# Kernel tuning notes

Hardware: AMD Instinct MI355X
Metric: run time of the kernel (lower is better)

Reference implementation:

```python
import jax, jax.numpy as jnp
import numpy as np

B, C, H, W = 64, 1, 1024, 1024
G, K, S = 64, 3, 2
HG0, HL = 512, 512
D_IN = K * G * G * C  # 12288


def setup_inputs() -> dict:
    key = jax.random.key(0)
    k1, k2, k3, k4, k5, k6 = jax.random.split(key, 6)
    x = jax.random.normal(k1, (B, C, H, W), dtype=jnp.float32)
    l_t_prev = jax.random.uniform(k2, (B, 2), dtype=jnp.float32, minval=-1.0, maxval=1.0)
    W1 = jax.random.normal(k3, (HG0, D_IN), dtype=jnp.float32) * 0.02
    W2 = jax.random.normal(k4, (HL, 2), dtype=jnp.float32) * 0.02
    W3 = jax.random.normal(k5, (HG0 + HL, HG0), dtype=jnp.float32) * 0.02
    W4 = jax.random.normal(k6, (HG0 + HL, HL), dtype=jnp.float32) * 0.02
    return {"x": x, "l_t_prev": l_t_prev, "W1": W1, "W2": W2, "W3": W3, "W4": W4}


def _extract_patch(x, coords, size):
    """Crop a size x size window per sample, centered at coords, zero-padded OOB,
    then avg-pool by factor size//G down to (B, C, G, G)."""
    r = size // G
    P = size // 2 + 1  # padding used by the torch code; makes every slice in-bounds
    xp = jnp.pad(x, ((0, 0), (0, 0), (P, P), (P, P)))
    sy = coords[:, 1] - size // 2 + P
    sx = coords[:, 0] - size // 2 + P

    def one(im, y0, x0):
        return jax.lax.dynamic_slice(im, (0, y0, x0), (C, size, size))

    p = jax.vmap(one)(xp, sy, sx)  # (B, C, size, size)
    if r > 1:
        p = p.reshape(B, C, G, r, G, r).mean(axis=(3, 5))  # avg_pool2d(kernel=r)
    return p


def _foveate(x, l):
    # denormalize: coords in [0, H], truncated to int
    coords = (0.5 * ((l + 1.0) * H)).astype(jnp.int32)  # (B, 2) as [x, y]
    patches = []
    size = G * S ** (K - 1)
    for _ in range(K):
        patches.append(_extract_patch(x, coords, size))  # (B, 1, G, G)
        size = size // S
    return jnp.concatenate(patches, axis=1)  # (B, K, G, G)


def reference(x, l_t_prev, W1, W2, W3, W4):
    phi = _foveate(x, l_t_prev)                      # (B, K, G, G)
    phi_flat = phi.reshape(phi.shape[0], -1)         # (B, K*G*G)
    h = jax.nn.leaky_relu(phi_flat @ W1.T)           # (B, HG0)
    l_out = jax.nn.leaky_relu(l_t_prev @ W2.T)       # computed but unused (as in source)
    what = h @ W3.T                                  # (B, HG0+HL)
    where = h @ W4.T                                 # fc4 applied to phi features (source quirk)
    g_t = jax.nn.leaky_relu(what + where)
    return g_t
```

## Files before the change

kernel.cpp:

```cpp
#include <hip/hip_runtime.h>
#include <hip/hip_bf16.h>

#define B_N 64
#define D_IN 12288
#define HG0 512
#define OUT_N 1024

#define KC1 16
#define DBLOCK1 768
#define DWAVE1 192

typedef __attribute__((ext_vector_type(8))) short bf16x8;
typedef __attribute__((ext_vector_type(4))) float f32x4;

static __device__ __forceinline__ short f2bf(float f) {
  __hip_bfloat16 h = __float2bfloat16(f);
  return *reinterpret_cast<short*>(&h);
}

__global__ __launch_bounds__(256) void foveate_kernel(
    const float* __restrict__ x, const float* __restrict__ l,
    short* __restrict__ phi) {
  int idx = blockIdx.x * 256 + threadIdx.x;
  int b = idx / D_IN;
  int d = idx - b * D_IN;
  int k = d >> 12;
  int rem = d & 4095;
  int gy = rem >> 6, gx = rem & 63;

  float lx = l[b * 2 + 0];
  float ly = l[b * 2 + 1];
  int cx = (int)(0.5f * ((lx + 1.0f) * 1024.0f));
  int cy = (int)(0.5f * ((ly + 1.0f) * 1024.0f));

  const float* xb = x + ((size_t)b << 20);
  float v;

  if (k == 0) {
    int y0 = cy - 128 + gy * 4;
    int x0 = cx - 128 + gx * 4;
    float s = 0.0f;
    #pragma unroll
    for (int dy = 0; dy < 4; ++dy) {
      int yy = y0 + dy;
      if ((unsigned)yy < 1024u) {
        const float* row = xb + ((size_t)yy << 10);
        #pragma unroll
        for (int dx = 0; dx < 4; ++dx) {
          int xx = x0 + dx;
          if ((unsigned)xx < 1024u) s += row[xx];
        }
      }
    }
    v = s * 0.0625f;
  } else if (k == 1) {
    int y0 = cy - 64 + gy * 2;
    int x0 = cx - 64 + gx * 2;
    float s = 0.0f;
    #pragma unroll
    for (int dy = 0; dy < 2; ++dy) {
      int yy = y0 + dy;
      if ((unsigned)yy < 1024u) {
        const float* row = xb + ((size_t)yy << 10);
        #pragma unroll
        for (int dx = 0; dx < 2; ++dx) {
          int xx = x0 + dx;
          if ((unsigned)xx < 1024u) s += row[xx];
        }
      }
    }
    v = s * 0.25f;
  } else {
    int yy = cy - 32 + gy;
    int xx = cx - 32 + gx;
    v = 0.0f;
    if ((unsigned)yy < 1024u && (unsigned)xx < 1024u) v = xb[((size_t)yy << 10) + xx];
  }
  phi[idx] = f2bf(v);
}

__global__ __launch_bounds__(256) void gemm1_kernel(
    const short* __restrict__ phi, const float* __restrict__ W1,
    float* __restrict__ partial1) {
  __shared__ float lds[4 * 16 * 64];
  int wave = threadIdx.x >> 6;
  int lane = threadIdx.x & 63;
  int lc = lane & 15;
  int kg = lane >> 4;
  int j0 = blockIdx.x * 16;
  int dbase = blockIdx.y * DBLOCK1 + wave * DWAVE1;

  f32x4 acc[4] = {{0,0,0,0},{0,0,0,0},{0,0,0,0},{0,0,0,0}};

  const float* wrow = W1 + (size_t)(j0 + lc) * D_IN + kg * 8;
  const short* prow = phi + kg * 8;

  #pragma unroll
  for (int ks = 0; ks < DWAVE1 / 32; ++ks) {
    int d0 = dbase + ks * 32;
    float4 wa = *(const float4*)(wrow + d0);
    float4 wb = *(const float4*)(wrow + d0 + 4);
    bf16x8 af;
    af[0] = f2bf(wa.x); af[1] = f2bf(wa.y); af[2] = f2bf(wa.z); af[3] = f2bf(wa.w);
    af[4] = f2bf(wb.x); af[5] = f2bf(wb.y); af[6] = f2bf(wb.z); af[7] = f2bf(wb.w);
    #pragma unroll
    for (int t = 0; t < 4; ++t) {
      bf16x8 bf = *(const bf16x8*)(prow + (size_t)(t * 16 + lc) * D_IN + d0);
      acc[t] = __builtin_amdgcn_mfma_f32_16x16x32_bf16(af, bf, acc[t], 0, 0, 0);
    }
  }

  #pragma unroll
  for (int t = 0; t < 4; ++t)
    #pragma unroll
    for (int r = 0; r < 4; ++r)
      lds[wave * 1024 + (kg * 4 + r) * 64 + t * 16 + lc] = acc[t][r];
  __syncthreads();

  float* pp = partial1 + (size_t)blockIdx.y * (HG0 * 64) + (size_t)j0 * 64;
  #pragma unroll
  for (int i = 0; i < 4; ++i) {
    int e = threadIdx.x + 256 * i;
    float s = lds[e] + lds[1024 + e] + lds[2048 + e] + lds[3072 + e];
    pp[e] = s;
  }
}

__global__ __launch_bounds__(256) void reduce1_kernel(
    const float* __restrict__ partial1, short* __restrict__ h) {
  int idx = blockIdx.x * 256 + threadIdx.x;
  float s = 0.0f;
  #pragma unroll
  for (int kc = 0; kc < KC1; ++kc) s += partial1[(size_t)kc * (HG0 * 64) + idx];
  float v = (s >= 0.0f) ? s : 0.01f * s;
  int j = idx >> 6, b = idx & 63;
  h[(size_t)b * HG0 + j] = f2bf(v);
}

__global__ __launch_bounds__(256) void gemm2_kernel(
    const short* __restrict__ h, const float* __restrict__ W3,
    const float* __restrict__ W4, float* __restrict__ out) {
  __shared__ float lds[4 * 1024];
  int wave = threadIdx.x >> 6;
  int lane = threadIdx.x & 63;
  int lc = lane & 15;
  int kg = lane >> 4;
  int o0 = blockIdx.x * 16;
  int jbase = wave * 128;

  f32x4 acc[4] = {{0,0,0,0},{0,0,0,0},{0,0,0,0},{0,0,0,0}};

  #pragma unroll
  for (int ks = 0; ks < 4; ++ks) {
    int j0 = jbase + ks * 32;
    const float* w3r = W3 + (size_t)(o0 + lc) * HG0 + j0 + kg * 8;
    const float* w4r = W4 + (size_t)(o0 + lc) * HG0 + j0 + kg * 8;
    float4 a3 = *(const float4*)w3r;
    float4 b3 = *(const float4*)(w3r + 4);
    float4 a4 = *(const float4*)w4r;
    float4 b4 = *(const float4*)(w4r + 4);
    bf16x8 bf;
    bf[0] = f2bf(a3.x + a4.x); bf[1] = f2bf(a3.y + a4.y);
    bf[2] = f2bf(a3.z + a4.z); bf[3] = f2bf(a3.w + a4.w);
    bf[4] = f2bf(b3.x + b4.x); bf[5] = f2bf(b3.y + b4.y);
    bf[6] = f2bf(b3.z + b4.z); bf[7] = f2bf(b3.w + b4.w);
    #pragma unroll
    for (int t = 0; t < 4; ++t) {
      bf16x8 af = *(const bf16x8*)(h + (size_t)(t * 16 + lc) * HG0 + j0 + kg * 8);
      acc[t] = __builtin_amdgcn_mfma_f32_16x16x32_bf16(af, bf, acc[t], 0, 0, 0);
    }
  }

  #pragma unroll
  for (int t = 0; t < 4; ++t)
    #pragma unroll
    for (int r = 0; r < 4; ++r)
      lds[wave * 1024 + t * 256 + kg * 64 + r * 16 + lc] = acc[t][r];
  __syncthreads();

  #pragma unroll
  for (int i = 0; i < 4; ++i) {
    int e = threadIdx.x + 256 * i;
    float s = lds[e] + lds[1024 + e] + lds[2048 + e] + lds[3072 + e];
    float v = (s >= 0.0f) ? s : 0.01f * s;
    int b = ((e >> 8) << 4) + (((e >> 6) & 3) << 2) + ((e >> 4) & 3);
    out[(size_t)b * OUT_N + o0 + (e & 15)] = v;
  }
}

extern "C" void kernel_launch(void* const* d_in, const int* in_sizes, int n_in,
                              void* d_out, int out_size, void* d_ws, size_t ws_size,
                              hipStream_t stream) {
  const float* x  = (const float*)d_in[0];
  const float* l  = (const float*)d_in[1];
  const float* W1 = (const float*)d_in[2];
  const float* W3 = (const float*)d_in[4];
  const float* W4 = (const float*)d_in[5];
  float* out = (float*)d_out;

  char* ws = (char*)d_ws;
  short* phi      = (short*)(ws);
  float* partial1 = (float*)(ws + (1u << 21));
  short* h        = (short*)(ws + (1u << 21) + (1u << 22));

  foveate_kernel<<<dim3((B_N * D_IN) / 256), dim3(256), 0, stream>>>(x, l, phi);
  gemm1_kernel<<<dim3(32, KC1), dim3(256), 0, stream>>>(phi, W1, partial1);
  reduce1_kernel<<<dim3((HG0 * 64) / 256), dim3(256), 0, stream>>>(partial1, h);
  gemm2_kernel<<<dim3(OUT_N / 16), dim3(256), 0, stream>>>(h, W3, W4, out);
}
```

Measured before the change: 34.36 us.

## Fuse split-K reduction into gemm1 via atomic counter, precombine W3+W4 in prep

The separate reduce kernel is removed. The last gemm1 block to finish each output tile, detected with an atomic counter and thread fences, now sums the split-K partials and writes the leaky-relu bf16 h. W3+W4 is summed and converted to bf16 once, inside the foveate launch, so gemm2 reads half the bytes and does no conversion. Split-K is doubled to 32 to put more blocks in flight, which doubles the partial traffic and adds the serial reduction tail in the last block of each tile.

```diff
diff --git a/kernel.cpp b/kernel.cpp
--- a/kernel.cpp
+++ b/kernel.cpp
@@ -6,9 +6,12 @@
 #define HG0 512
 #define OUT_N 1024
 
-#define KC1 16
-#define DBLOCK1 768
-#define DWAVE1 192
+#define KC1 32
+#define DBLOCK1 384
+#define DWAVE1 96
+
+#define NFOV 3072
+#define NW34 512
 
 typedef __attribute__((ext_vector_type(8))) short bf16x8;
 typedef __attribute__((ext_vector_type(4))) float f32x4;
@@ -18,10 +21,24 @@
   return *reinterpret_cast<short*>(&h);
 }
 
-__global__ __launch_bounds__(256) void foveate_kernel(
+__global__ __launch_bounds__(256) void prep_kernel(
     const float* __restrict__ x, const float* __restrict__ l,
-    short* __restrict__ phi) {
-  int idx = blockIdx.x * 256 + threadIdx.x;
+    const float* __restrict__ W3, const float* __restrict__ W4,
+    short* __restrict__ phi, short* __restrict__ w34, int* __restrict__ cnt) {
+  int bx = blockIdx.x;
+  if (bx >= NFOV) {
+    int e = (bx - NFOV) * 1024 + threadIdx.x * 4;
+    float4 a = *(const float4*)(W3 + e);
+    float4 b = *(const float4*)(W4 + e);
+    short4 o;
+    o.x = f2bf(a.x + b.x); o.y = f2bf(a.y + b.y);
+    o.z = f2bf(a.z + b.z); o.w = f2bf(a.w + b.w);
+    *(short4*)(w34 + e) = o;
+    if (bx == NFOV && threadIdx.x < 32) cnt[threadIdx.x] = 0;
+    return;
+  }
+
+  int idx = bx * 256 + threadIdx.x;
   int b = idx / D_IN;
   int d = idx - b * D_IN;
   int k = d >> 12;
@@ -81,8 +98,9 @@
 
 __global__ __launch_bounds__(256) void gemm1_kernel(
     const short* __restrict__ phi, const float* __restrict__ W1,
-    float* __restrict__ partial1) {
+    float* __restrict__ partial1, short* __restrict__ h, int* __restrict__ cnt) {
   __shared__ float lds[4 * 16 * 64];
+  __shared__ int lastflag;
   int wave = threadIdx.x >> 6;
   int lane = threadIdx.x & 63;
   int lc = lane & 15;
@@ -121,25 +139,35 @@
   #pragma unroll
   for (int i = 0; i < 4; ++i) {
     int e = threadIdx.x + 256 * i;
-    float s = lds[e] + lds[1024 + e] + lds[2048 + e] + lds[3072 + e];
-    pp[e] = s;
-  }
-}
-
-__global__ __launch_bounds__(256) void reduce1_kernel(
-    const float* __restrict__ partial1, short* __restrict__ h) {
-  int idx = blockIdx.x * 256 + threadIdx.x;
-  float s = 0.0f;
-  #pragma unroll
-  for (int kc = 0; kc < KC1; ++kc) s += partial1[(size_t)kc * (HG0 * 64) + idx];
-  float v = (s >= 0.0f) ? s : 0.01f * s;
-  int j = idx >> 6, b = idx & 63;
-  h[(size_t)b * HG0 + j] = f2bf(v);
+    pp[e] = lds[e] + lds[1024 + e] + lds[2048 + e] + lds[3072 + e];
+  }
+
+  __threadfence();
+  __syncthreads();
+  if (threadIdx.x == 0) {
+    int t = atomicAdd(&cnt[blockIdx.x], 1);
+    lastflag = (t == KC1 - 1);
+  }
+  __syncthreads();
+  if (!lastflag) return;
+  __threadfence();
+
+  const float* pbase = partial1 + (size_t)j0 * 64;
+  #pragma unroll
+  for (int i = 0; i < 4; ++i) {
+    int e = threadIdx.x + 256 * i;
+    float s = 0.0f;
+    #pragma unroll
+    for (int kc = 0; kc < KC1; ++kc) s += pbase[(size_t)kc * (HG0 * 64) + e];
+    float v = (s >= 0.0f) ? s : 0.01f * s;
+    int j = j0 + (e >> 6), b = e & 63;
+    h[(size_t)b * HG0 + j] = f2bf(v);
+  }
 }
 
 __global__ __launch_bounds__(256) void gemm2_kernel(
-    const short* __restrict__ h, const float* __restrict__ W3,
-    const float* __restrict__ W4, float* __restrict__ out) {
+    const short* __restrict__ h, const short* __restrict__ w34,
+    float* __restrict__ out) {
   __shared__ float lds[4 * 1024];
   int wave = threadIdx.x >> 6;
   int lane = threadIdx.x & 63;
@@ -153,17 +181,7 @@
   #pragma unroll
   for (int ks = 0; ks < 4; ++ks) {
     int j0 = jbase + ks * 32;
-    const float* w3r = W3 + (size_t)(o0 + lc) * HG0 + j0 + kg * 8;
-    const float* w4r = W4 + (size_t)(o0 + lc) * HG0 + j0 + kg * 8;
-    float4 a3 = *(const float4*)w3r;
-    float4 b3 = *(const float4*)(w3r + 4);
-    float4 a4 = *(const float4*)w4r;
-    float4 b4 = *(const float4*)(w4r + 4);
-    bf16x8 bf;
-    bf[0] = f2bf(a3.x + a4.x); bf[1] = f2bf(a3.y + a4.y);
-    bf[2] = f2bf(a3.z + a4.z); bf[3] = f2bf(a3.w + a4.w);
-    bf[4] = f2bf(b3.x + b4.x); bf[5] = f2bf(b3.y + b4.y);
-    bf[6] = f2bf(b3.z + b4.z); bf[7] = f2bf(b3.w + b4.w);
+    bf16x8 bf = *(const bf16x8*)(w34 + (size_t)(o0 + lc) * HG0 + j0 + kg * 8);
     #pragma unroll
     for (int t = 0; t < 4; ++t) {
       bf16x8 af = *(const bf16x8*)(h + (size_t)(t * 16 + lc) * HG0 + j0 + kg * 8);
@@ -200,11 +218,12 @@
 
   char* ws = (char*)d_ws;
   short* phi      = (short*)(ws);
-  float* partial1 = (float*)(ws + (1u << 21));
-  short* h        = (short*)(ws + (1u << 21) + (1u << 22));
-
-  foveate_kernel<<<dim3((B_N * D_IN) / 256), dim3(256), 0, stream>>>(x, l, phi);
-  gemm1_kernel<<<dim3(32, KC1), dim3(256), 0, stream>>>(phi, W1, partial1);
-  reduce1_kernel<<<dim3((HG0 * 64) / 256), dim3(256), 0, stream>>>(partial1, h);
-  gemm2_kernel<<<dim3(OUT_N / 16), dim3(256), 0, stream>>>(h, W3, W4, out);
-}
+  float* partial1 = (float*)(ws + (2u << 20));
+  short* h        = (short*)(ws + (6u << 20));
+  short* w34      = (short*)(ws + (7u << 20));
+  int*   cnt      = (int*)(ws + (9u << 20));
+
+  prep_kernel<<<dim3(NFOV + NW34), dim3(256), 0, stream>>>(x, l, W3, W4, phi, w34, cnt);
+  gemm1_kernel<<<dim3(32, KC1), dim3(256), 0, stream>>>(phi, W1, partial1, h, cnt);
+  gemm2_kernel<<<dim3(OUT_N / 16), dim3(256), 0, stream>>>(h, w34, out);
+}
```

After: 132.3 us. 285% more time.
